# Kernel optimization log

Hardware: AMD Instinct MI355X
Metric: run time of the kernel (lower is better)

Reference implementation:

```python
import jax, jax.numpy as jnp
import numpy as np

D = 768
CTX = 64


def ln(x, g, b, eps=1e-5):
    m = x.mean(-1, keepdims=True)
    v = jnp.mean((x - m) ** 2, -1, keepdims=True)
    return (x - m) / jnp.sqrt(v + eps) * g + b


def setup_inputs() -> dict:
    key = jax.random.key(0)
    ks = jax.random.split(key, 16)
    B, N = 16, 1024
    w = lambda k, shape: jax.random.normal(k, shape, dtype=jnp.float32) * 0.02
    return {
        'comps': jax.random.normal(ks[0], (8, B, N, D), jnp.float32),
        'geometric_context': jax.random.normal(ks[1], (B, N, D), jnp.float32),
        'question_features': jax.random.normal(ks[2], (B, D), jnp.float32),
        'spatial_mask': jax.random.randint(ks[3], (B,), 0, 2) > 0,
        'gp_w1': w(ks[4], (D, D // 2)), 'gp_b1': jnp.zeros((D // 2,)),
        'gp_g1': jnp.ones((D // 2,)), 'gp_be1': jnp.zeros((D // 2,)),
        'gp_w2': w(ks[5], (D // 2, CTX)), 'gp_b2': jnp.zeros((CTX,)),
        'swp_w1': w(ks[6], (CTX + D, 256)), 'swp_b1': jnp.zeros((256,)),
        'swp_g1': jnp.ones((256,)), 'swp_be1': jnp.zeros((256,)),
        'swp_w2': w(ks[7], (256, 128)), 'swp_b2': jnp.zeros((128,)),
        'swp_g2': jnp.ones((128,)), 'swp_be2': jnp.zeros((128,)),
        'swp_w3': w(ks[8], (128, 8)), 'swp_b3': jnp.zeros((8,)),
        'sw1': w(ks[9], (4, D + CTX, D)), 'sb1': jnp.zeros((4, D)),
        'sg1': jnp.ones((4, D)), 'sbe1': jnp.zeros((4, D)),
        'sw2': w(ks[10], (4, D, D)), 'sb2': jnp.zeros((4, D)),
        'sg2': jnp.ones((4, D)), 'sbe2': jnp.zeros((4, D)),
        'rw1': w(ks[11], (4, D + CTX, D)), 'rb1': jnp.zeros((4, D)),
        'rg1': jnp.ones((4, D)), 'rbe1': jnp.zeros((4, D)),
        'rw2': w(ks[12], (4, D, D)), 'rb2': jnp.zeros((4, D)),
    }


def reference(comps, geometric_context, question_features, spatial_mask,
              gp_w1, gp_b1, gp_g1, gp_be1, gp_w2, gp_b2,
              swp_w1, swp_b1, swp_g1, swp_be1, swp_w2, swp_b2, swp_g2, swp_be2, swp_w3, swp_b3,
              sw1, sb1, sg1, sbe1, sw2, sb2, sg2, sbe2,
              rw1, rb1, rg1, rbe1, rw2, rb2):
    B, N = geometric_context.shape[:2]
    # geometric_processor on mean-pooled context -> [B, 64]
    gcc = jax.nn.relu(ln(geometric_context.mean(1) @ gp_w1 + gp_b1, gp_g1, gp_be1)) @ gp_w2 + gp_b2
    # spatial_weight_predictor -> softmax weights [B, 8]
    wi = jnp.concatenate([gcc, question_features], -1)
    h = jax.nn.gelu(ln(wi @ swp_w1 + swp_b1, swp_g1, swp_be1), approximate=False)
    h = jax.nn.gelu(ln(h @ swp_w2 + swp_b2, swp_g2, swp_be2), approximate=False)
    aw = jax.nn.softmax(h @ swp_w3 + swp_b3, -1)
    # expanded context; non-spatial samples use 0.1-scaled context for spatial-set comps
    ctx = jnp.broadcast_to(gcc[:, None, :], (B, N, CTX))
    ctx_s = ctx * jnp.where(spatial_mask, 1.0, 0.1)[:, None, None]
    # strong enhancers (GELU, second LN): P_unique(0), V_unique(1), PV(3), PT(5) - all spatial-set
    xs = jnp.concatenate([comps[jnp.array([0, 1, 3, 5])],
                          jnp.broadcast_to(ctx_s, (4, B, N, CTX))], -1)
    h = jax.nn.gelu(ln(jnp.einsum('kbnd,kdf->kbnf', xs, sw1) + sb1[:, None, None, :],
                       sg1[:, None, None, :], sbe1[:, None, None, :]), approximate=False)
    ys = ln(jnp.einsum('kbnd,kdf->kbnf', h, sw2) + sb2[:, None, None, :],
            sg2[:, None, None, :], sbe2[:, None, None, :])
    # ReLU enhancers (moderate/minimal share structure): TV(4, scaled ctx), T_unique(2), redundant(6), higher(7)
    ctx_r = jnp.stack([ctx_s, ctx, ctx, ctx], 0)
    xr = jnp.concatenate([comps[jnp.array([4, 2, 6, 7])], ctx_r], -1)
    h = jax.nn.relu(ln(jnp.einsum('kbnd,kdf->kbnf', xr, rw1) + rb1[:, None, None, :],
                       rg1[:, None, None, :], rbe1[:, None, None, :]))
    yr = jnp.einsum('kbnd,kdf->kbnf', h, rw2) + rb2[:, None, None, :]
    # non-spatial components pass through when spatial_mask is False
    m = spatial_mask[:, None, None]
    out = jnp.stack([
        ys[0],                              # P_unique
        ys[1],                              # V_unique
        jnp.where(m, yr[1], comps[2]),      # T_unique
        ys[2],                              # PV_synergy
        yr[0],                              # TV_synergy
        ys[3],                              # PT_synergy
        jnp.where(m, yr[2], comps[6]),      # redundant
        jnp.where(m, yr[3], comps[7]),      # higher_synergy
    ], 0)
    return out, aw
```

## Files before the change

### kernel.cpp

```cpp
#include <hip/hip_runtime.h>
#include <math.h>

#define MT 16384
#define DD 768
#define AW_OFF ((size_t)8 * MT * DD)

typedef __attribute__((ext_vector_type(8))) short short8;
typedef __attribute__((ext_vector_type(4))) float f32x4;
typedef __attribute__((ext_vector_type(4))) float fv4;
typedef __attribute__((ext_vector_type(4))) unsigned int u32x4;

#define OFF_W1T 0ULL
#define OFF_W2T 10223616ULL
#define OFF_Z1  19660800ULL
#define OFF_Z2  220987392ULL
#define OFF_P1  321675264ULL
#define OFF_P2  324820992ULL
#define OFF_ST1 326393856ULL
#define OFF_ST2 327442432ULL
#define OFF_GP  327966720ULL
#define OFF_GM  328359936ULL
#define OFF_CXS 328409088ULL
#define OFF_CXU 328411136ULL
#define OFF_A1  335544320ULL

static __device__ __forceinline__ unsigned short f2bf(float f) {
  unsigned u = __float_as_uint(f);
  u += 0x7fffu + ((u >> 16) & 1u);
  return (unsigned short)(u >> 16);
}
static __device__ __forceinline__ float bf2f(unsigned short h) {
  return __uint_as_float(((unsigned)h) << 16);
}
static __device__ __forceinline__ unsigned pk2(float lo, float hi) {
  return (unsigned)f2bf(lo) | ((unsigned)f2bf(hi) << 16);
}
static __device__ __forceinline__ float gelu_t(float y) {
  float y2 = y * y;
  float c = fmaf(y2, 0.0713548163f, 1.59576912161f);
  float e = __expf(-y * c);
  return y / (1.0f + e);
}
static __device__ __forceinline__ void gload_lds16(const void* g, void* l) {
  __builtin_amdgcn_global_load_lds(
      (const __attribute__((address_space(1))) void*)g,
      (__attribute__((address_space(3))) void*)l, 16, 0, 0);
}

__global__ void transpose_cvt(const float* sw1, const float* rw1,
                              const float* sw2, const float* rw2,
                              unsigned short* w1T, unsigned short* w2T) {
  __shared__ float t[32][33];
  const int z = blockIdx.z;
  int R; const float* sp; unsigned short* dp;
  if (z < 8) {
    R = 832;
    sp = ((z < 4) ? sw1 : rw1) + (size_t)(z & 3) * 832 * DD;
    dp = w1T + (size_t)z * DD * 832;
  } else {
    R = 768;
    int zz = z - 8;
    sp = ((zz < 4) ? sw2 : rw2) + (size_t)(zz & 3) * DD * DD;
    dp = w2T + (size_t)zz * DD * DD;
  }
  const int r0 = blockIdx.x * 32, c0 = blockIdx.y * 32;
  if (r0 >= R) return;
  const int tx = threadIdx.x & 31, ty = threadIdx.x >> 5;
#pragma unroll
  for (int i = 0; i < 4; i++) {
    int r = ty + i * 8;
    t[r][tx] = sp[(size_t)(r0 + r) * DD + c0 + tx];
  }
  __syncthreads();
#pragma unroll
  for (int i = 0; i < 4; i++) {
    int cc = ty + i * 8;
    dp[(size_t)(c0 + cc) * R + r0 + tx] = f2bf(t[tx][cc]);
  }
}

__global__ void colmean1(const float* __restrict__ geo, float* __restrict__ gp) {
  const int b = blockIdx.z, yc = blockIdx.y;
  const int col = blockIdx.x * 256 + threadIdx.x;
  const float* p = geo + (size_t)b * 1024 * DD + (size_t)yc * 128 * DD + col;
  float s = 0.f;
  for (int n = 0; n < 128; ++n) s += p[(size_t)n * DD];
  gp[((size_t)b * 8 + yc) * DD + col] = s;
}
__global__ void colmean2(const float* __restrict__ gp, float* __restrict__ gm) {
  const int b = blockIdx.y;
  const int col = blockIdx.x * 256 + threadIdx.x;
  float s = 0.f;
#pragma unroll
  for (int i = 0; i < 8; ++i) s += gp[((size_t)b * 8 + i) * DD + col];
  gm[(size_t)b * DD + col] = s * (1.0f / 1024.0f);
}

static __device__ float2 blk_sum2(float a, float b, float* red) {
  const int tid = threadIdx.x;
  __syncthreads();
  red[tid] = a; red[512 + tid] = b;
  if (tid < 128) { red[384 + tid] = 0.f; red[512 + 384 + tid] = 0.f; }
  __syncthreads();
  for (int s = 256; s > 0; s >>= 1) {
    if (tid < s) { red[tid] += red[tid + s]; red[512 + tid] += red[512 + tid + s]; }
    __syncthreads();
  }
  return make_float2(red[0], red[512]);
}

__global__ void small_mlp(
    const float* __restrict__ gc_mean, const float* __restrict__ qf,
    const int* __restrict__ mask,
    const float* __restrict__ gp_w1, const float* __restrict__ gp_b1,
    const float* __restrict__ gp_g1, const float* __restrict__ gp_be1,
    const float* __restrict__ gp_w2, const float* __restrict__ gp_b2,
    const float* __restrict__ swp_w1, const float* __restrict__ swp_b1,
    const float* __restrict__ swp_g1, const float* __restrict__ swp_be1,
    const float* __restrict__ swp_w2, const float* __restrict__ swp_b2,
    const float* __restrict__ swp_g2, const float* __restrict__ swp_be2,
    const float* __restrict__ swp_w3, const float* __restrict__ swp_b3,
    unsigned short* __restrict__ ctxs, unsigned short* __restrict__ ctxu,
    float* __restrict__ aw)
{
  __shared__ float gm[768];
  __shared__ float buf[832];
  __shared__ float tmp[384];
  __shared__ float red[1024];
  const int b = blockIdx.x, tid = threadIdx.x;

  for (int i = tid; i < 768; i += 384) gm[i] = gc_mean[b * 768 + i];
  __syncthreads();

  float z = gp_b1[tid];
  for (int k = 0; k < 768; k++) z += gm[k] * gp_w1[k * 384 + tid];
  float2 s = blk_sum2(z, z * z, red);
  {
    float mean = s.x * (1.f / 384.f);
    float rinv = rsqrtf(s.y * (1.f / 384.f) - mean * mean + 1e-5f);
    float y = (z - mean) * rinv * gp_g1[tid] + gp_be1[tid];
    tmp[tid] = fmaxf(y, 0.f);
  }
  __syncthreads();

  if (tid < 64) {
    float g = gp_b2[tid];
    for (int k = 0; k < 384; k++) g += tmp[k] * gp_w2[k * 64 + tid];
    float sc = (mask[b] != 0) ? 1.0f : 0.1f;
    ctxs[b * 64 + tid] = f2bf(g * sc);
    ctxu[b * 64 + tid] = f2bf(g);
    buf[tid] = g;
  }
  for (int i = tid; i < 768; i += 384) buf[64 + i] = qf[b * 768 + i];
  __syncthreads();

  float z1 = 0.f;
  if (tid < 256) {
    z1 = swp_b1[tid];
    for (int k = 0; k < 832; k++) z1 += buf[k] * swp_w1[k * 256 + tid];
  }
  s = blk_sum2(z1, z1 * z1, red);
  {
    float mean = s.x * (1.f / 256.f);
    float rinv = rsqrtf(s.y * (1.f / 256.f) - mean * mean + 1e-5f);
    if (tid < 256) {
      float y = (z1 - mean) * rinv * swp_g1[tid] + swp_be1[tid];
      tmp[tid] = 0.5f * y * (1.f + erff(y * 0.7071067811865476f));
    }
  }
  __syncthreads();

  float z2 = 0.f;
  if (tid < 128) {
    z2 = swp_b2[tid];
    for (int k = 0; k < 256; k++) z2 += tmp[k] * swp_w2[k * 128 + tid];
  }
  s = blk_sum2(z2, z2 * z2, red);
  {
    float mean = s.x * (1.f / 128.f);
    float rinv = rsqrtf(s.y * (1.f / 128.f) - mean * mean + 1e-5f);
    if (tid < 128) {
      float y = (z2 - mean) * rinv * swp_g2[tid] + swp_be2[tid];
      tmp[tid] = 0.5f * y * (1.f + erff(y * 0.7071067811865476f));
    }
  }
  __syncthreads();

  if (tid < 8) {
    float z3 = swp_b3[tid];
    for (int k = 0; k < 128; k++) z3 += tmp[k] * swp_w3[k * 8 + tid];
    buf[tid] = z3;
  }
  __syncthreads();
  if (tid < 8) {
    float mx = buf[0];
    for (int k = 1; k < 8; k++) mx = fmaxf(mx, buf[k]);
    float ssum = 0.f;
    for (int k = 0; k < 8; k++) ssum += expf(buf[k] - mx);
    aw[b * 8 + tid] = expf(buf[tid] - mx) / ssum;
  }
}

__global__ void stats_k(const float2* __restrict__ part, float2* __restrict__ st,
                        int nr) {
  int i = blockIdx.x * 256 + threadIdx.x;
  if (i >= nr) return;
  float2 p0 = part[i], p1 = part[nr + i], p2 = part[2 * nr + i];
  float s1 = p0.x + p1.x + p2.x, s2 = p0.y + p1.y + p2.y;
  float mean = s1 * (1.f / 768.f);
  float var = s2 * (1.f / 768.f) - mean * mean;
  float rinv = rsqrtf(var + 1e-5f);
  st[i] = make_float2(rinv, -mean * rinv);
}

__global__ __launch_bounds__(512, 4)
void gemm1_k(const float* __restrict__ comps,
             const unsigned short* __restrict__ cxs,
             const unsigned short* __restrict__ cxu,
             const unsigned short* __restrict__ w1T,
             const float* __restrict__ sb1, const float* __restrict__ rb1,
             unsigned short* __restrict__ z1,
             float2* __restrict__ part1,
             const int* __restrict__ mask)
{
  __shared__ __align__(16) unsigned short As[2][4096];
  __shared__ __align__(16) unsigned short Bs[2][8192];
  __shared__ float pscr[4][128][2];
  constexpr int NT = 26;

  const int id = blockIdx.x;
  const int x = id & 7, j = id >> 3;
  const int br_nt = j >> 4;
  const int mt = ((j & 15) << 3) | x;
  const int nt = br_nt % 3;
  const int br = br_nt / 3;
  const int m0 = mt * 128, n0 = nt * 256;
  const int b = m0 >> 10;
  if (br >= 5 && mask[b] == 0) return;

  const int ci = (0x76245310u >> (br * 4)) & 15;
  const float* afp = comps + (size_t)ci * MT * DD + (size_t)m0 * DD;
  const unsigned short* ctxp = ((br <= 4) ? cxs : cxu) + b * 64;
  const unsigned short* wT = w1T + (size_t)br * DD * 832 + (size_t)n0 * 832;

  const int tid = threadIdx.x;
  const int w = tid >> 6, lane = tid & 63, llo = lane & 15, lhi = lane >> 4;
  const int wm = w & 1, wn = w >> 1;

  const int arow = tid >> 2, ap = tid & 3;
  const int aslot = (arow * 32 + ((ap ^ ((arow >> 1) & 3)) << 3));
  const float* asrc = afp + (size_t)arow * DD + ap * 8;
  const unsigned short* csrc = ctxp + ap * 8;

  const int q = lane & 3, rrB = w * 16 + (lane >> 2);
  const int swqB = q ^ ((rrB >> 1) & 3);
  const unsigned short* bsrc0 = wT + (size_t)rrB * 832 + swqB * 8;
  const unsigned short* bsrc1 = wT + (size_t)(128 + rrB) * 832 + swqB * 8;

  f32x4 acc[4][4];
#pragma unroll
  for (int mf = 0; mf < 4; ++mf)
#pragma unroll
    for (int nf = 0; nf < 4; ++nf) acc[mf][nf] = (f32x4)0.0f;

  struct St { u32x4 q0, q1; };

  auto issueB = [&](int kt, int s) {
    gload_lds16(bsrc0 + (size_t)kt * 32, &Bs[s][w * 512]);
    gload_lds16(bsrc1 + (size_t)kt * 32, &Bs[s][4096 + w * 512]);
  };
  auto loadA = [&](int kt) -> St {
    St s;
    if (kt < 24) {
      const u32x4* p = (const u32x4*)(asrc + kt * 32);
      s.q0 = p[0]; s.q1 = p[1];
    } else {
      s.q0 = *(const u32x4*)(csrc + (kt - 24) * 32);
      s.q1 = s.q0;
    }
    return s;
  };
  auto commitA = [&](const St& s, int kt, int sl) {
    u32x4 v;
    if (kt < 24) {
      v[0] = pk2(__uint_as_float(s.q0[0]), __uint_as_float(s.q0[1]));
      v[1] = pk2(__uint_as_float(s.q0[2]), __uint_as_float(s.q0[3]));
      v[2] = pk2(__uint_as_float(s.q1[0]), __uint_as_float(s.q1[1]));
      v[3] = pk2(__uint_as_float(s.q1[2]), __uint_as_float(s.q1[3]));
    } else {
      v = s.q0;
    }
    *(u32x4*)&As[sl][aslot] = v;
  };

  const int aswz = (lhi ^ ((llo >> 1) & 3)) << 3;
  const int arow0 = (wm * 64 + llo) * 32 + aswz;
  const int brow0 = (wn * 64 + llo) * 32 + aswz;
  auto compute = [&](int sl) {
    short8 afr[4];
#pragma unroll
    for (int mf = 0; mf < 4; ++mf)
      afr[mf] = *(const short8*)&As[sl][arow0 + mf * 512];
#pragma unroll
    for (int nf = 0; nf < 4; ++nf) {
      short8 bfr = *(const short8*)&Bs[sl][brow0 + nf * 512];
#pragma unroll
      for (int mf = 0; mf < 4; ++mf)
        acc[mf][nf] = __builtin_amdgcn_mfma_f32_16x16x32_bf16(afr[mf], bfr, acc[mf][nf], 0, 0, 0);
    }
  };

  issueB(0, 0);
  {
    St s0 = loadA(0);
    commitA(s0, 0, 0);
  }
  asm volatile("s_waitcnt lgkmcnt(0)" ::: "memory");
  __builtin_amdgcn_sched_barrier(0);
  __builtin_amdgcn_s_barrier();

#pragma unroll 1
  for (int t = 0; t < NT; ++t) {
    const int cur = t & 1, nxt = cur ^ 1;
    const bool more = (t + 1 < NT);
    St sn;
    if (more) {
      issueB(t + 1, nxt);
      sn = loadA(t + 1);
    }
    __builtin_amdgcn_sched_barrier(0);
    compute(cur);
    __builtin_amdgcn_sched_barrier(0);
    if (more) commitA(sn, t + 1, nxt);
    asm volatile("s_waitcnt lgkmcnt(0)" ::: "memory");
    __builtin_amdgcn_sched_barrier(0);
    __builtin_amdgcn_s_barrier();
  }

  const float* bias = ((br < 4) ? sb1 : rb1) + (br & 3) * DD;
  unsigned short* zo = z1 + (size_t)br * MT * DD + (size_t)m0 * DD;
  const int n0w = n0 + wn * 64;
  float bia[4];
#pragma unroll
  for (int nf = 0; nf < 4; ++nf) bia[nf] = bias[n0w + nf * 16 + llo];
#pragma unroll
  for (int mf = 0; mf < 4; ++mf) {
#pragma unroll
    for (int r = 0; r < 4; ++r) {
      float zz[4]; float s1v = 0.f, s2v = 0.f;
#pragma unroll
      for (int nf = 0; nf < 4; ++nf) {
        float zv = acc[mf][nf][r] + bia[nf];
        zz[nf] = zv; s1v += zv; s2v += zv * zv;
      }
      const int rloc = wm * 64 + mf * 16 + lhi * 4 + r;
      const size_t rowoff = (size_t)rloc * DD;
#pragma unroll
      for (int nf = 0; nf < 4; ++nf) {
        float zon = __shfl_xor(zz[nf], 1);
        if ((llo & 1) == 0)
          *(unsigned*)&zo[rowoff + n0w + nf * 16 + llo] = pk2(zz[nf], zon);
      }
#pragma unroll
      for (int d = 1; d < 16; d <<= 1) {
        s1v += __shfl_xor(s1v, d); s2v += __shfl_xor(s2v, d);
      }
      if (llo == 0) { pscr[wn][rloc][0] = s1v; pscr[wn][rloc][1] = s2v; }
    }
  }
  __syncthreads();
  if (tid < 128) {
    float a = 0.f, c = 0.f;
#pragma unroll
    for (int qq = 0; qq < 4; ++qq) { a += pscr[qq][tid][0]; c += pscr[qq][tid][1]; }
    part1[(size_t)nt * (8 * MT) + (size_t)br * MT + m0 + tid] = make_float2(a, c);
  }
}

__global__ void act1_k(const unsigned short* __restrict__ z1,
                       const float2* __restrict__ st1,
                       const float* __restrict__ sg1, const float* __restrict__ sbe1,
                       const float* __restrict__ rg1, const float* __restrict__ rbe1,
                       const int* __restrict__ mask,
                       unsigned short* __restrict__ a1)
{
  const int tid = threadIdx.x;
  const int rowg = blockIdx.x * 8 + (tid >> 5);
  const int l = tid & 31;
  const int br = rowg >> 14;
  const int r = rowg & 16383;
  const int b = r >> 10;
  if (br >= 5 && mask[b] == 0) return;
  const bool isg = (br < 4);
  const float* g  = (isg ? sg1  + br * DD : rg1  + (br - 4) * DD);
  const float* be = (isg ? sbe1 + br * DD : rbe1 + (br - 4) * DD);
  const float2 stv = st1[rowg];
  const unsigned short* zp = z1 + (size_t)rowg * DD;
  unsigned short* op = a1 + (size_t)rowg * DD;
#pragma unroll
  for (int c = 0; c < 3; ++c) {
    const int col = l * 8 + c * 256;
    u32x4 zv = *(const u32x4*)(zp + col);
    fv4 ga = *(const fv4*)(g + col), gb = *(const fv4*)(g + col + 4);
    fv4 ba = *(const fv4*)(be + col), bb = *(const fv4*)(be + col + 4);
    float y[8];
#pragma unroll
    for (int wd = 0; wd < 2; ++wd) {
      y[2*wd]   = fmaf(fmaf(bf2f((unsigned short)(zv[wd] & 0xffffu)), stv.x, stv.y), ga[2*wd], ba[2*wd]);
      y[2*wd+1] = fmaf(fmaf(bf2f((unsigned short)(zv[wd] >> 16)), stv.x, stv.y), ga[2*wd+1], ba[2*wd+1]);
      y[4+2*wd]   = fmaf(fmaf(bf2f((unsigned short)(zv[wd+2] & 0xffffu)), stv.x, stv.y), gb[2*wd], bb[2*wd]);
      y[4+2*wd+1] = fmaf(fmaf(bf2f((unsigned short)(zv[wd+2] >> 16)), stv.x, stv.y), gb[2*wd+1], bb[2*wd+1]);
    }
    u32x4 ov;
#pragma unroll
    for (int wd = 0; wd < 4; ++wd) {
      float y0 = y[2*wd], y1 = y[2*wd+1];
      if (isg) { y0 = gelu_t(y0); y1 = gelu_t(y1); }
      else     { y0 = fmaxf(y0, 0.f); y1 = fmaxf(y1, 0.f); }
      ov[wd] = pk2(y0, y1);
    }
    *(u32x4*)(op + col) = ov;
  }
}

__global__ __launch_bounds__(512, 4)
void gemm2_k(const float* __restrict__ comps,
             const unsigned short* __restrict__ a1,
             const unsigned short* __restrict__ w2T,
             const float* __restrict__ sb2, const float* __restrict__ rb2,
             unsigned short* __restrict__ z2,
             float2* __restrict__ part2,
             float* __restrict__ outp,
             const int* __restrict__ mask)
{
  __shared__ __align__(16) unsigned short As[3][4096];
  __shared__ __align__(16) unsigned short Bs[3][8192];
  __shared__ float pscr[4][128][2];
  constexpr int NT = 24;

  const int id = blockIdx.x;
  const int x = id & 7, j = id >> 3;
  const int br_nt = j >> 4;
  const int mt = ((j & 15) << 3) | x;
  const int nt = br_nt % 3;
  const int br = br_nt / 3;
  const int m0 = mt * 128, n0 = nt * 256;
  const int b = m0 >> 10;
  const int ci = (0x76245310u >> (br * 4)) & 15;
  const int tid = threadIdx.x;

  if (br >= 5 && mask[b] == 0) {
    const float* cs = comps + (size_t)ci * MT * DD + (size_t)m0 * DD + n0;
    float* cd = outp + (size_t)ci * MT * DD + (size_t)m0 * DD + n0;
#pragma unroll 1
    for (int k = 0; k < 16; ++k) {
      int idx = tid + k * 512;
      int r2 = idx >> 6, c4 = (idx & 63) * 4;
      *(fv4*)(cd + (size_t)r2 * DD + c4) = *(const fv4*)(cs + (size_t)r2 * DD + c4);
    }
    return;
  }

  const unsigned short* az = a1 + (size_t)br * MT * DD + (size_t)m0 * DD;
  const unsigned short* wT = w2T + (size_t)br * DD * DD + (size_t)n0 * DD;

  const int w = tid >> 6, lane = tid & 63, llo = lane & 15, lhi = lane >> 4;
  const int wm = w & 1, wn = w >> 1;
  const int q = lane & 3, rrB = w * 16 + (lane >> 2);
  const int swqB = q ^ ((rrB >> 1) & 3);

  const unsigned short* asrcD = az + (size_t)rrB * DD + swqB * 8;
  const unsigned short* bsrc0 = wT + (size_t)rrB * DD + swqB * 8;
  const unsigned short* bsrc1 = wT + (size_t)(128 + rrB) * DD + swqB * 8;

  f32x4 acc[4][4];
#pragma unroll
  for (int mf = 0; mf < 4; ++mf)
#pragma unroll
    for (int nf = 0; nf < 4; ++nf) acc[mf][nf] = (f32x4)0.0f;

  auto issueT = [&](int kt, int s) {
    gload_lds16(asrcD + (size_t)kt * 32, &As[s][w * 512]);
    gload_lds16(bsrc0 + (size_t)kt * 32, &Bs[s][w * 512]);
    gload_lds16(bsrc1 + (size_t)kt * 32, &Bs[s][4096 + w * 512]);
  };

  const int aswz = (lhi ^ ((llo >> 1) & 3)) << 3;
  const int arow0 = (wm * 64 + llo) * 32 + aswz;
  const int brow0 = (wn * 64 + llo) * 32 + aswz;
  auto compute = [&](int sl) {
    short8 afr[4];
#pragma unroll
    for (int mf = 0; mf < 4; ++mf)
      afr[mf] = *(const short8*)&As[sl][arow0 + mf * 512];
#pragma unroll
    for (int nf = 0; nf < 4; ++nf) {
      short8 bfr = *(const short8*)&Bs[sl][brow0 + nf * 512];
#pragma unroll
      for (int mf = 0; mf < 4; ++mf)
        acc[mf][nf] = __builtin_amdgcn_mfma_f32_16x16x32_bf16(afr[mf], bfr, acc[mf][nf], 0, 0, 0);
    }
  };

  issueT(0, 0);
  issueT(1, 1);
  asm volatile("s_waitcnt vmcnt(3)" ::: "memory");
  __builtin_amdgcn_sched_barrier(0);
  __builtin_amdgcn_s_barrier();

  int sl = 0;
#pragma unroll 1
  for (int t = 0; t < NT; ++t) {
    int sl2 = sl + 2; if (sl2 >= 3) sl2 -= 3;
    const bool more = (t + 2 < NT);
    if (more) issueT(t + 2, sl2);
    __builtin_amdgcn_sched_barrier(0);
    compute(sl);
    if (more) asm volatile("s_waitcnt vmcnt(3)" ::: "memory");
    else      asm volatile("s_waitcnt vmcnt(0)" ::: "memory");
    asm volatile("s_waitcnt lgkmcnt(0)" ::: "memory");
    __builtin_amdgcn_sched_barrier(0);
    __builtin_amdgcn_s_barrier();
    ++sl; if (sl == 3) sl = 0;
  }

  const int n0w = n0 + wn * 64;
  const float* bias = ((br < 4) ? sb2 : rb2) + (br & 3) * DD;
  float bia[4];
#pragma unroll
  for (int nf = 0; nf < 4; ++nf) bia[nf] = bias[n0w + nf * 16 + llo];

  if (br < 4) {
    unsigned short* zo = z2 + (size_t)br * MT * DD + (size_t)m0 * DD;
#pragma unroll
    for (int mf = 0; mf < 4; ++mf) {
#pragma unroll
      for (int r = 0; r < 4; ++r) {
        float zz[4]; float s1v = 0.f, s2v = 0.f;
#pragma unroll
        for (int nf = 0; nf < 4; ++nf) {
          float zv = acc[mf][nf][r] + bia[nf];
          zz[nf] = zv; s1v += zv; s2v += zv * zv;
        }
        const int rloc = wm * 64 + mf * 16 + lhi * 4 + r;
        const size_t rowoff = (size_t)rloc * DD;
#pragma unroll
        for (int nf = 0; nf < 4; ++nf) {
          float zon = __shfl_xor(zz[nf], 1);
          if ((llo & 1) == 0)
            *(unsigned*)&zo[rowoff + n0w + nf * 16 + llo] = pk2(zz[nf], zon);
        }
#pragma unroll
        for (int d = 1; d < 16; d <<= 1) {
          s1v += __shfl_xor(s1v, d); s2v += __shfl_xor(s2v, d);
        }
        if (llo == 0) { pscr[wn][rloc][0] = s1v; pscr[wn][rloc][1] = s2v; }
      }
    }
    __syncthreads();
    if (tid < 128) {
      float a = 0.f, c = 0.f;
#pragma unroll
      for (int qq = 0; qq < 4; ++qq) { a += pscr[qq][tid][0]; c += pscr[qq][tid][1]; }
      part2[(size_t)nt * (4 * MT) + (size_t)br * MT + m0 + tid] = make_float2(a, c);
    }
  } else {
    float* fo = outp + (size_t)ci * MT * DD + (size_t)m0 * DD;
#pragma unroll
    for (int mf = 0; mf < 4; ++mf) {
#pragma unroll
      for (int r = 0; r < 4; ++r) {
        const int rloc = wm * 64 + mf * 16 + lhi * 4 + r;
        const size_t rowoff = (size_t)rloc * DD;
#pragma unroll
        for (int nf = 0; nf < 4; ++nf)
          fo[rowoff + n0w + nf * 16 + llo] = acc[mf][nf][r] + bia[nf];
      }
    }
  }
}

__global__ void finish_s(const unsigned short* __restrict__ z2,
                         const float2* __restrict__ st2,
                         const float* __restrict__ sg2,
                         const float* __restrict__ sbe2,
                         float* __restrict__ outp)
{
  const int tid = threadIdx.x;
  const int rowg = blockIdx.x * 8 + (tid >> 5);
  const int l = tid & 31;
  const int br = rowg >> 14;
  const int r = rowg & 16383;
  const int ci = (0x5310u >> (br * 4)) & 15;
  const unsigned short* zp = z2 + (size_t)rowg * DD;
  float* op = outp + (size_t)ci * MT * DD + (size_t)r * DD;
  const float2 stv = st2[rowg];
  const float* g = sg2 + br * DD;
  const float* be = sbe2 + br * DD;
#pragma unroll
  for (int c = 0; c < 3; ++c) {
    const int col = l * 8 + c * 256;
    u32x4 zv = *(const u32x4*)(zp + col);
    fv4 ga = *(const fv4*)(g + col), gb = *(const fv4*)(g + col + 4);
    fv4 ba = *(const fv4*)(be + col), bb = *(const fv4*)(be + col + 4);
    fv4 o0, o1;
#pragma unroll
    for (int wd = 0; wd < 2; ++wd) {
      o0[2 * wd]     = fmaf(fmaf(bf2f((unsigned short)(zv[wd] & 0xffffu)), stv.x, stv.y), ga[2 * wd], ba[2 * wd]);
      o0[2 * wd + 1] = fmaf(fmaf(bf2f((unsigned short)(zv[wd] >> 16)), stv.x, stv.y), ga[2 * wd + 1], ba[2 * wd + 1]);
      o1[2 * wd]     = fmaf(fmaf(bf2f((unsigned short)(zv[wd + 2] & 0xffffu)), stv.x, stv.y), gb[2 * wd], bb[2 * wd]);
      o1[2 * wd + 1] = fmaf(fmaf(bf2f((unsigned short)(zv[wd + 2] >> 16)), stv.x, stv.y), gb[2 * wd + 1], bb[2 * wd + 1]);
    }
    *(fv4*)(op + col) = o0;
    *(fv4*)(op + col + 4) = o1;
  }
}

extern "C" void kernel_launch(void* const* d_in, const int* in_sizes, int n_in,
                              void* d_out, int out_size, void* d_ws, size_t ws_size,
                              hipStream_t stream)
{
  (void)in_sizes; (void)n_in; (void)out_size; (void)ws_size;
  const float* comps  = (const float*)d_in[0];
  const float* geo    = (const float*)d_in[1];
  const float* qf     = (const float*)d_in[2];
  const int*   mask   = (const int*)d_in[3];
  const float* gp_w1  = (const float*)d_in[4];
  const float* gp_b1  = (const float*)d_in[5];
  const float* gp_g1  = (const float*)d_in[6];
  const float* gp_be1 = (const float*)d_in[7];
  const float* gp_w2  = (const float*)d_in[8];
  const float* gp_b2  = (const float*)d_in[9];
  const float* swp_w1 = (const float*)d_in[10];
  const float* swp_b1 = (const float*)d_in[11];
  const float* swp_g1 = (const float*)d_in[12];
  const float* swp_be1= (const float*)d_in[13];
  const float* swp_w2 = (const float*)d_in[14];
  const float* swp_b2 = (const float*)d_in[15];
  const float* swp_g2 = (const float*)d_in[16];
  const float* swp_be2= (const float*)d_in[17];
  const float* swp_w3 = (const float*)d_in[18];
  const float* swp_b3 = (const float*)d_in[19];
  const float* sw1 = (const float*)d_in[20];
  const float* sb1 = (const float*)d_in[21];
  const float* sg1 = (const float*)d_in[22];
  const float* sbe1= (const float*)d_in[23];
  const float* sw2 = (const float*)d_in[24];
  const float* sb2 = (const float*)d_in[25];
  const float* sg2 = (const float*)d_in[26];
  const float* sbe2= (const float*)d_in[27];
  const float* rw1 = (const float*)d_in[28];
  const float* rb1 = (const float*)d_in[29];
  const float* rg1 = (const float*)d_in[30];
  const float* rbe1= (const float*)d_in[31];
  const float* rw2 = (const float*)d_in[32];
  const float* rb2 = (const float*)d_in[33];
  float* out = (float*)d_out;

  char* ws = (char*)d_ws;
  unsigned short* w1T = (unsigned short*)(ws + OFF_W1T);
  unsigned short* w2T = (unsigned short*)(ws + OFF_W2T);
  unsigned short* z1  = (unsigned short*)(ws + OFF_Z1);
  unsigned short* z2  = (unsigned short*)(ws + OFF_Z2);
  float2* part1 = (float2*)(ws + OFF_P1);
  float2* part2 = (float2*)(ws + OFF_P2);
  float2* st1   = (float2*)(ws + OFF_ST1);
  float2* st2   = (float2*)(ws + OFF_ST2);
  float* gpart  = (float*)(ws + OFF_GP);
  float* gmean  = (float*)(ws + OFF_GM);
  unsigned short* cxs = (unsigned short*)(ws + OFF_CXS);
  unsigned short* cxu = (unsigned short*)(ws + OFF_CXU);
  unsigned short* a1  = (unsigned short*)(ws + OFF_A1);

  transpose_cvt<<<dim3(26, 24, 16), 256, 0, stream>>>(sw1, rw1, sw2, rw2, w1T, w2T);
  colmean1<<<dim3(3, 8, 16), 256, 0, stream>>>(geo, gpart);
  colmean2<<<dim3(3, 16), 256, 0, stream>>>(gpart, gmean);
  small_mlp<<<16, 384, 0, stream>>>(gmean, qf, mask,
      gp_w1, gp_b1, gp_g1, gp_be1, gp_w2, gp_b2,
      swp_w1, swp_b1, swp_g1, swp_be1, swp_w2, swp_b2, swp_g2, swp_be2,
      swp_w3, swp_b3, cxs, cxu, out + AW_OFF);

  gemm1_k<<<3072, 512, 0, stream>>>(comps, cxs, cxu, w1T, sb1, rb1, z1, part1, mask);
  stats_k<<<512, 256, 0, stream>>>(part1, st1, 8 * MT);
  act1_k<<<16384, 256, 0, stream>>>(z1, st1, sg1, sbe1, rg1, rbe1, mask, a1);
  gemm2_k<<<3072, 512, 0, stream>>>(comps, a1, w2T, sb2, rb2, z2, part2, out, mask);
  stats_k<<<256, 256, 0, stream>>>(part2, st2, 4 * MT);
  finish_s<<<8192, 256, 0, stream>>>(z2, st2, sg2, sbe2, out);
}
```

Measured before the change: 774.7 us.

## Fold context columns into per-batch bias and pre-convert comps to bf16

The per-batch context columns of the first enhancer GEMM are folded into a per-(branch, batch) bias by a new small kernel, ctxbias_k. This shortens the GEMM's K loop from 832 to 768 and removes the context A-tile path. Comps are converted to bf16 once in a separate pass, so gemm1 can stream both A and B tiles with asynchronous global-to-LDS loads in a three-stage pipeline, replacing the register-staged fp32 convert. The trade-off is an extra full read and write of the 8x16384x768 comps tensor and a larger workspace.

```diff
diff --git a/kernel.cpp b/kernel.cpp
--- a/kernel.cpp
+++ b/kernel.cpp
@@ -11,18 +11,19 @@
 typedef __attribute__((ext_vector_type(4))) unsigned int u32x4;
 
 #define OFF_W1T 0ULL
-#define OFF_W2T 10223616ULL
+#define OFF_W2T 9437184ULL
 #define OFF_Z1  19660800ULL
 #define OFF_Z2  220987392ULL
-#define OFF_P1  321675264ULL
-#define OFF_P2  324820992ULL
-#define OFF_ST1 326393856ULL
-#define OFF_ST2 327442432ULL
-#define OFF_GP  327966720ULL
-#define OFF_GM  328359936ULL
-#define OFF_CXS 328409088ULL
-#define OFF_CXU 328411136ULL
+#define OFF_P1  321650688ULL
+#define OFF_P2  327942144ULL
+#define OFF_ST1 331087872ULL
+#define OFF_ST2 332136448ULL
+#define OFF_GP  332660736ULL
+#define OFF_GM  333053952ULL
+#define OFF_CXF 333103104ULL
+#define OFF_B1X 333111296ULL
 #define OFF_A1  335544320ULL
+#define OFF_CB  536870912ULL
 
 static __device__ __forceinline__ unsigned short f2bf(float f) {
   unsigned u = __float_as_uint(f);
@@ -47,24 +48,35 @@
       (__attribute__((address_space(3))) void*)l, 16, 0, 0);
 }
 
+__global__ void cvt_comps(const float* __restrict__ c,
+                          unsigned short* __restrict__ cb, long n8) {
+  long i = (long)blockIdx.x * blockDim.x + threadIdx.x;
+  const long stride = (long)gridDim.x * blockDim.x;
+  for (; i < n8; i += stride) {
+    const fv4* p = (const fv4*)(c + i * 8);
+    fv4 a = p[0], b = p[1];
+    u32x4 v;
+    v[0] = pk2(a[0], a[1]); v[1] = pk2(a[2], a[3]);
+    v[2] = pk2(b[0], b[1]); v[3] = pk2(b[2], b[3]);
+    *(u32x4*)(cb + i * 8) = v;
+  }
+}
+
 __global__ void transpose_cvt(const float* sw1, const float* rw1,
                               const float* sw2, const float* rw2,
                               unsigned short* w1T, unsigned short* w2T) {
   __shared__ float t[32][33];
   const int z = blockIdx.z;
-  int R; const float* sp; unsigned short* dp;
+  const float* sp; unsigned short* dp;
   if (z < 8) {
-    R = 832;
     sp = ((z < 4) ? sw1 : rw1) + (size_t)(z & 3) * 832 * DD;
-    dp = w1T + (size_t)z * DD * 832;
+    dp = w1T + (size_t)z * DD * DD;
   } else {
-    R = 768;
     int zz = z - 8;
     sp = ((zz < 4) ? sw2 : rw2) + (size_t)(zz & 3) * DD * DD;
     dp = w2T + (size_t)zz * DD * DD;
   }
   const int r0 = blockIdx.x * 32, c0 = blockIdx.y * 32;
-  if (r0 >= R) return;
   const int tx = threadIdx.x & 31, ty = threadIdx.x >> 5;
 #pragma unroll
   for (int i = 0; i < 4; i++) {
@@ -75,7 +87,7 @@
 #pragma unroll
   for (int i = 0; i < 4; i++) {
     int cc = ty + i * 8;
-    dp[(size_t)(c0 + cc) * R + r0 + tx] = f2bf(t[tx][cc]);
+    dp[(size_t)(c0 + cc) * DD + r0 + tx] = f2bf(t[tx][cc]);
   }
 }
 
@@ -120,7 +132,7 @@
     const float* __restrict__ swp_w2, const float* __restrict__ swp_b2,
     const float* __restrict__ swp_g2, const float* __restrict__ swp_be2,
     const float* __restrict__ swp_w3, const float* __restrict__ swp_b3,
-    unsigned short* __restrict__ ctxs, unsigned short* __restrict__ ctxu,
+    float* __restrict__ cxfs, float* __restrict__ cxfu,
     float* __restrict__ aw)
 {
   __shared__ float gm[768];
@@ -147,8 +159,8 @@
     float g = gp_b2[tid];
     for (int k = 0; k < 384; k++) g += tmp[k] * gp_w2[k * 64 + tid];
     float sc = (mask[b] != 0) ? 1.0f : 0.1f;
-    ctxs[b * 64 + tid] = f2bf(g * sc);
-    ctxu[b * 64 + tid] = f2bf(g);
+    cxfs[b * 64 + tid] = g * sc;
+    cxfu[b * 64 + tid] = g;
     buf[tid] = g;
   }
   for (int i = tid; i < 768; i += 384) buf[64 + i] = qf[b * 768 + i];
@@ -201,12 +213,38 @@
   }
 }
 
+__global__ void ctxbias_k(const float* __restrict__ cxfs,
+                          const float* __restrict__ cxfu,
+                          const float* __restrict__ sw1, const float* __restrict__ rw1,
+                          const float* __restrict__ sb1, const float* __restrict__ rb1,
+                          float* __restrict__ b1x)
+{
+  const int br = blockIdx.x, b = blockIdx.y, tid = threadIdx.x;
+  __shared__ float cf[64];
+  if (tid < 64) cf[tid] = ((br <= 4) ? cxfs : cxfu)[b * 64 + tid];
+  __syncthreads();
+  const float* W = ((br < 4) ? sw1 + (size_t)br * 832 * DD
+                             : rw1 + (size_t)(br - 4) * 832 * DD) + (size_t)768 * DD;
+  const float* bb = (br < 4) ? sb1 + br * DD : rb1 + (br - 4) * DD;
+#pragma unroll
+  for (int jj = 0; jj < 3; ++jj) {
+    const int f = tid + jj * 256;
+    float s = bb[f];
+    for (int k = 0; k < 64; ++k) s += cf[k] * W[(size_t)k * DD + f];
+    b1x[((size_t)br * 16 + b) * DD + f] = s;
+  }
+}
+
 __global__ void stats_k(const float2* __restrict__ part, float2* __restrict__ st,
                         int nr) {
   int i = blockIdx.x * 256 + threadIdx.x;
   if (i >= nr) return;
-  float2 p0 = part[i], p1 = part[nr + i], p2 = part[2 * nr + i];
-  float s1 = p0.x + p1.x + p2.x, s2 = p0.y + p1.y + p2.y;
+  float s1 = 0.f, s2 = 0.f;
+#pragma unroll
+  for (int s = 0; s < 3; ++s) {
+    float2 p = part[(size_t)s * nr + i];
+    s1 += p.x; s2 += p.y;
+  }
   float mean = s1 * (1.f / 768.f);
   float var = s2 * (1.f / 768.f) - mean * mean;
   float rinv = rsqrtf(var + 1e-5f);
@@ -214,19 +252,17 @@
 }
 
 __global__ __launch_bounds__(512, 4)
-void gemm1_k(const float* __restrict__ comps,
-             const unsigned short* __restrict__ cxs,
-             const unsigned short* __restrict__ cxu,
+void gemm1_k(const unsigned short* __restrict__ compsb,
              const unsigned short* __restrict__ w1T,
-             const float* __restrict__ sb1, const float* __restrict__ rb1,
+             const float* __restrict__ b1x,
              unsigned short* __restrict__ z1,
              float2* __restrict__ part1,
              const int* __restrict__ mask)
 {
-  __shared__ __align__(16) unsigned short As[2][4096];
-  __shared__ __align__(16) unsigned short Bs[2][8192];
+  __shared__ __align__(16) unsigned short As[3][4096];
+  __shared__ __align__(16) unsigned short Bs[3][8192];
   __shared__ float pscr[4][128][2];
-  constexpr int NT = 26;
+  constexpr int NT = 24;
 
   const int id = blockIdx.x;
   const int x = id & 7, j = id >> 3;
@@ -239,23 +275,18 @@
   if (br >= 5 && mask[b] == 0) return;
 
   const int ci = (0x76245310u >> (br * 4)) & 15;
-  const float* afp = comps + (size_t)ci * MT * DD + (size_t)m0 * DD;
-  const unsigned short* ctxp = ((br <= 4) ? cxs : cxu) + b * 64;
-  const unsigned short* wT = w1T + (size_t)br * DD * 832 + (size_t)n0 * 832;
+  const unsigned short* az = compsb + (size_t)ci * MT * DD + (size_t)m0 * DD;
+  const unsigned short* wT = w1T + (size_t)br * DD * DD + (size_t)n0 * DD;
 
   const int tid = threadIdx.x;
   const int w = tid >> 6, lane = tid & 63, llo = lane & 15, lhi = lane >> 4;
   const int wm = w & 1, wn = w >> 1;
-
-  const int arow = tid >> 2, ap = tid & 3;
-  const int aslot = (arow * 32 + ((ap ^ ((arow >> 1) & 3)) << 3));
-  const float* asrc = afp + (size_t)arow * DD + ap * 8;
-  const unsigned short* csrc = ctxp + ap * 8;
-
   const int q = lane & 3, rrB = w * 16 + (lane >> 2);
   const int swqB = q ^ ((rrB >> 1) & 3);
-  const unsigned short* bsrc0 = wT + (size_t)rrB * 832 + swqB * 8;
-  const unsigned short* bsrc1 = wT + (size_t)(128 + rrB) * 832 + swqB * 8;
+
+  const unsigned short* asrcD = az + (size_t)rrB * DD + swqB * 8;
+  const unsigned short* bsrc0 = wT + (size_t)rrB * DD + swqB * 8;
+  const unsigned short* bsrc1 = wT + (size_t)(128 + rrB) * DD + swqB * 8;
 
   f32x4 acc[4][4];
 #pragma unroll
@@ -263,34 +294,10 @@
 #pragma unroll
     for (int nf = 0; nf < 4; ++nf) acc[mf][nf] = (f32x4)0.0f;
 
-  struct St { u32x4 q0, q1; };
-
-  auto issueB = [&](int kt, int s) {
+  auto issueT = [&](int kt, int s) {
+    gload_lds16(asrcD + (size_t)kt * 32, &As[s][w * 512]);
     gload_lds16(bsrc0 + (size_t)kt * 32, &Bs[s][w * 512]);
     gload_lds16(bsrc1 + (size_t)kt * 32, &Bs[s][4096 + w * 512]);
-  };
-  auto loadA = [&](int kt) -> St {
-    St s;
-    if (kt < 24) {
-      const u32x4* p = (const u32x4*)(asrc + kt * 32);
-      s.q0 = p[0]; s.q1 = p[1];
-    } else {
-      s.q0 = *(const u32x4*)(csrc + (kt - 24) * 32);
-      s.q1 = s.q0;
-    }
-    return s;
-  };
-  auto commitA = [&](const St& s, int kt, int sl) {
-    u32x4 v;
-    if (kt < 24) {
-      v[0] = pk2(__uint_as_float(s.q0[0]), __uint_as_float(s.q0[1]));
-      v[1] = pk2(__uint_as_float(s.q0[2]), __uint_as_float(s.q0[3]));
-      v[2] = pk2(__uint_as_float(s.q1[0]), __uint_as_float(s.q1[1]));
-      v[3] = pk2(__uint_as_float(s.q1[2]), __uint_as_float(s.q1[3]));
-    } else {
-      v = s.q0;
-    }
-    *(u32x4*)&As[sl][aslot] = v;
   };
 
   const int aswz = (lhi ^ ((llo >> 1) & 3)) << 3;
@@ -310,34 +317,29 @@
     }
   };
 
-  issueB(0, 0);
-  {
-    St s0 = loadA(0);
-    commitA(s0, 0, 0);
-  }
-  asm volatile("s_waitcnt lgkmcnt(0)" ::: "memory");
+  issueT(0, 0);
+  issueT(1, 1);
+  asm volatile("s_waitcnt vmcnt(3)" ::: "memory");
   __builtin_amdgcn_sched_barrier(0);
   __builtin_amdgcn_s_barrier();
 
+  int sc = 0;
 #pragma unroll 1
   for (int t = 0; t < NT; ++t) {
-    const int cur = t & 1, nxt = cur ^ 1;
-    const bool more = (t + 1 < NT);
-    St sn;
-    if (more) {
-      issueB(t + 1, nxt);
-      sn = loadA(t + 1);
-    }
+    int s2 = sc + 2; if (s2 >= 3) s2 -= 3;
+    const bool more = (t + 2 < NT);
+    if (more) issueT(t + 2, s2);
     __builtin_amdgcn_sched_barrier(0);
-    compute(cur);
-    __builtin_amdgcn_sched_barrier(0);
-    if (more) commitA(sn, t + 1, nxt);
+    compute(sc);
+    if (more) asm volatile("s_waitcnt vmcnt(3)" ::: "memory");
+    else      asm volatile("s_waitcnt vmcnt(0)" ::: "memory");
     asm volatile("s_waitcnt lgkmcnt(0)" ::: "memory");
     __builtin_amdgcn_sched_barrier(0);
     __builtin_amdgcn_s_barrier();
-  }
-
-  const float* bias = ((br < 4) ? sb1 : rb1) + (br & 3) * DD;
+    ++sc; if (sc == 3) sc = 0;
+  }
+
+  const float* bias = b1x + ((size_t)br * 16 + b) * DD;
   unsigned short* zo = z1 + (size_t)br * MT * DD + (size_t)m0 * DD;
   const int n0w = n0 + wn * 64;
   float bia[4];
@@ -508,20 +510,20 @@
   __builtin_amdgcn_sched_barrier(0);
   __builtin_amdgcn_s_barrier();
 
-  int sl = 0;
+  int sc = 0;
 #pragma unroll 1
   for (int t = 0; t < NT; ++t) {
-    int sl2 = sl + 2; if (sl2 >= 3) sl2 -= 3;
+    int s2 = sc + 2; if (s2 >= 3) s2 -= 3;
     const bool more = (t + 2 < NT);
-    if (more) issueT(t + 2, sl2);
+    if (more) issueT(t + 2, s2);
     __builtin_amdgcn_sched_barrier(0);
-    compute(sl);
+    compute(sc);
     if (more) asm volatile("s_waitcnt vmcnt(3)" ::: "memory");
     else      asm volatile("s_waitcnt vmcnt(0)" ::: "memory");
     asm volatile("s_waitcnt lgkmcnt(0)" ::: "memory");
     __builtin_amdgcn_sched_barrier(0);
     __builtin_amdgcn_s_barrier();
-    ++sl; if (sl == 3) sl = 0;
+    ++sc; if (sc == 3) sc = 0;
   }
 
   const int n0w = n0 + wn * 64;
@@ -668,19 +670,23 @@
   float2* st2   = (float2*)(ws + OFF_ST2);
   float* gpart  = (float*)(ws + OFF_GP);
   float* gmean  = (float*)(ws + OFF_GM);
-  unsigned short* cxs = (unsigned short*)(ws + OFF_CXS);
-  unsigned short* cxu = (unsigned short*)(ws + OFF_CXU);
-  unsigned short* a1  = (unsigned short*)(ws + OFF_A1);
-
-  transpose_cvt<<<dim3(26, 24, 16), 256, 0, stream>>>(sw1, rw1, sw2, rw2, w1T, w2T);
+  float* cxfs   = (float*)(ws + OFF_CXF);
+  float* cxfu   = (float*)(ws + OFF_CXF + 4096);
+  float* b1x    = (float*)(ws + OFF_B1X);
+  unsigned short* a1     = (unsigned short*)(ws + OFF_A1);
+  unsigned short* compsb = (unsigned short*)(ws + OFF_CB);
+
+  cvt_comps<<<2048, 256, 0, stream>>>(comps, compsb, (long)8 * MT * DD / 8);
+  transpose_cvt<<<dim3(24, 24, 16), 256, 0, stream>>>(sw1, rw1, sw2, rw2, w1T, w2T);
   colmean1<<<dim3(3, 8, 16), 256, 0, stream>>>(geo, gpart);
   colmean2<<<dim3(3, 16), 256, 0, stream>>>(gpart, gmean);
   small_mlp<<<16, 384, 0, stream>>>(gmean, qf, mask,
       gp_w1, gp_b1, gp_g1, gp_be1, gp_w2, gp_b2,
       swp_w1, swp_b1, swp_g1, swp_be1, swp_w2, swp_b2, swp_g2, swp_be2,
-      swp_w3, swp_b3, cxs, cxu, out + AW_OFF);
-
-  gemm1_k<<<3072, 512, 0, stream>>>(comps, cxs, cxu, w1T, sb1, rb1, z1, part1, mask);
+      swp_w3, swp_b3, cxfs, cxfu, out + AW_OFF);
+  ctxbias_k<<<dim3(8, 16), 256, 0, stream>>>(cxfs, cxfu, sw1, rw1, sb1, rb1, b1x);
+
+  gemm1_k<<<3072, 512, 0, stream>>>(compsb, w1T, b1x, z1, part1, mask);
   stats_k<<<512, 256, 0, stream>>>(part1, st1, 8 * MT);
   act1_k<<<16384, 256, 0, stream>>>(z1, st1, sg1, sbe1, rg1, rbe1, mask, a1);
   gemm2_k<<<3072, 512, 0, stream>>>(comps, a1, w2T, sb2, rb2, z2, part2, out, mask);
```

Result: slower. 855.3 us (+10.4%).
